# Kernel tuning notes

Hardware: AMD Instinct MI355X
Metric: run time of the kernel (lower is better)

## Reference

```python
import jax, jax.numpy as jnp
import numpy as np

B, T, C = 4, 2048, 2048
H = 16
DK = C // H // 2          # head_k_dim = 64
DV = C // H               # head_v_dim = 128
KEY_DIM = H * DK          # 1024
VAL_DIM = H * DV          # 2048
CONV = 4                  # short conv kernel size
SCALE = DK ** -0.5


def setup_inputs() -> dict:
    key = jax.random.key(0)
    ks = jax.random.split(key, 12)
    s = 0.02
    rn = lambda k, shape, sc: (jax.random.normal(k, shape) * sc).astype(jnp.float32)
    return dict(
        x=jax.random.normal(ks[0], (B, T, C), jnp.float32),
        qk_w=rn(ks[1], (2 * KEY_DIM, C), s),
        vg_w=rn(ks[2], (2 * VAL_DIM, C), s),
        o_w=rn(ks[3], (C, VAL_DIM), s),
        a_w=rn(ks[4], (H, C), s),
        b_w=rn(ks[5], (H, C), s),
        b_bias=jnp.zeros((H,), jnp.float32),
        beta_bias=jnp.linspace(-1.5, 1.5, H).astype(jnp.float32),
        A_log=jnp.log(jax.random.uniform(ks[6], (H,), minval=2.0, maxval=8.0)).astype(jnp.float32),
        dt_bias=rn(ks[7], (H,), 0.1),
        q_conv_w=rn(ks[8], (KEY_DIM, 1, CONV), 0.3),
        k_conv_w=rn(ks[9], (KEY_DIM, 1, CONV), 0.3),
        v_conv_w=rn(ks[10], (VAL_DIM, 1, CONV), 0.3),
    )


def _causal_dwconv_silu(x, w):
    # x: [B,T,Ch], w: [Ch,1,K]; Conv1d(groups=Ch, padding=K-1) truncated to T == causal conv
    y = jax.lax.conv_general_dilated(
        jnp.transpose(x, (0, 2, 1)), w, (1,), [(w.shape[-1] - 1, 0)],
        dimension_numbers=('NCH', 'OIH', 'NCH'), feature_group_count=x.shape[-1])
    return jax.nn.silu(jnp.transpose(y, (0, 2, 1)))


def _l2norm(x, eps=1e-6):
    return x * jax.lax.rsqrt(jnp.sum(x * x, axis=-1, keepdims=True) + eps)


def _gated_delta_rule(q, k, v, g, beta):
    # q,k: [B,T,H,DK], v: [B,T,H,DV], g,beta: [B,T,H]
    q = _l2norm(q) * SCALE
    k = _l2norm(k)
    # time-major for scan
    qt, kt, vt = (jnp.moveaxis(a, 1, 0) for a in (q, k, v))
    gt, bt = jnp.moveaxis(g, 1, 0), jnp.moveaxis(beta, 1, 0)

    def step(S, inp):
        q_t, k_t, v_t, g_t, b_t = inp          # S: [B,H,DK,DV]
        S = S * jnp.exp(g_t)[..., None, None]  # forget gate
        mem = jnp.einsum('bhk,bhkv->bhv', k_t, S)
        delta = (v_t - mem) * b_t[..., None]   # beta-scaled delta update
        S = S + jnp.einsum('bhk,bhv->bhkv', k_t, delta)
        o_t = jnp.einsum('bhk,bhkv->bhv', q_t, S)
        return S, o_t

    S0 = jnp.zeros((q.shape[0], H, DK, DV), q.dtype)
    _, o = jax.lax.scan(step, S0, (qt, kt, vt, gt, bt))
    return jnp.moveaxis(o, 0, 1)  # [B,T,H,DV]


def reference(x, qk_w, vg_w, o_w, a_w, b_w, b_bias, beta_bias, A_log, dt_bias,
              q_conv_w, k_conv_w, v_conv_w):
    qk = x @ qk_w.T
    vg = x @ vg_w.T
    q, k = qk[..., :KEY_DIM], qk[..., KEY_DIM:]
    v, g_out = vg[..., :VAL_DIM], vg[..., VAL_DIM:]

    q = _causal_dwconv_silu(q, q_conv_w)
    k = _causal_dwconv_silu(k, k_conv_w)
    v = _causal_dwconv_silu(v, v_conv_w)

    Bm, Tm = x.shape[0], x.shape[1]
    q = q.reshape(Bm, Tm, H, DK)
    k = k.reshape(Bm, Tm, H, DK)
    v = v.reshape(Bm, Tm, H, DV)

    beta = jax.nn.sigmoid(x @ b_w.T + b_bias + beta_bias) * 2.0          # [B,T,H]
    g = -jnp.exp(A_log) * jax.nn.softplus(x @ a_w.T + dt_bias)           # [B,T,H]

    o = _gated_delta_rule(q, k, v, g, beta)                              # [B,T,H,DV]

    eps = jnp.finfo(o.dtype).eps
    o = o * jax.lax.rsqrt(jnp.mean(o * o, axis=-1, keepdims=True) + eps)  # rms_norm (no weight)
    o = o * jax.nn.silu(g_out.reshape(Bm, Tm, H, DV))
    return o.reshape(Bm, Tm, VAL_DIM) @ o_w.T
```

## Files before the change

kernel.cpp:

```cpp
#include <hip/hip_runtime.h>
#include <hip/hip_bf16.h>
#include <stdint.h>

#define B_ 4
#define T_ 2048
#define C_ 2048
#define H_ 16
#define DK_ 64
#define DV_ 128
#define BT_ (B_ * T_)

typedef __attribute__((ext_vector_type(8))) __bf16 bf16x8;
typedef __attribute__((ext_vector_type(4))) float f32x4;

__device__ __forceinline__ unsigned short f2bf(float f) {
    union { float f; uint32_t u; } v; v.f = f;
    uint32_t u = v.u;
    uint32_t r = u + 0x7FFFu + ((u >> 16) & 1u);
    return (unsigned short)(r >> 16);
}
__device__ __forceinline__ float bf2f(unsigned short h) {
    union { uint32_t u; float f; } v; v.u = ((uint32_t)h) << 16; return v.f;
}
__device__ __forceinline__ float siluf(float x) { return x / (1.f + expf(-x)); }

__device__ __forceinline__ float dpp_xor1_add(float x) {
    int t = __builtin_amdgcn_update_dpp(0, __float_as_int(x), 0xB1, 0xF, 0xF, true);
    return x + __int_as_float(t);
}
__device__ __forceinline__ float dpp_xor2_add(float x) {
    int t = __builtin_amdgcn_update_dpp(0, __float_as_int(x), 0x4E, 0xF, 0xF, true);
    return x + __int_as_float(t);
}

__device__ __forceinline__ void split_hl(float x, unsigned short& h, unsigned short& l) {
    unsigned short hu = f2bf(x);
    float lo = x - bf2f(hu);
    h = hu;
    l = (unsigned short)(__float_as_uint(lo) >> 16);
}

__global__ void cast_split_k(const float* __restrict__ in,
                             unsigned short* __restrict__ oh, unsigned short* __restrict__ ol, int n4) {
    int i = blockIdx.x * blockDim.x + threadIdx.x;
    if (i >= n4) return;
    float4 v = ((const float4*)in)[i];
    ushort4 h, l;
    split_hl(v.x, h.x, l.x); split_hl(v.y, h.y, l.y);
    split_hl(v.z, h.z, l.z); split_hl(v.w, h.w, l.w);
    ((ushort4*)oh)[i] = h;
    ((ushort4*)ol)[i] = l;
}

__global__ void cast_plain_k(const float* __restrict__ in, unsigned short* __restrict__ out, int n4) {
    int i = blockIdx.x * blockDim.x + threadIdx.x;
    if (i >= n4) return;
    float4 v = ((const float4*)in)[i];
    ushort4 o;
    o.x = f2bf(v.x); o.y = f2bf(v.y); o.z = f2bf(v.z); o.w = f2bf(v.w);
    ((ushort4*)out)[i] = o;
}

__device__ __forceinline__ void gld_lds16(const unsigned short* gptr,
                                          unsigned short* lds_base) {
    __builtin_amdgcn_global_load_lds(
        (const __attribute__((address_space(1))) uint32_t*)(uintptr_t)gptr,
        (__attribute__((address_space(3))) uint32_t*)(uint32_t)(uintptr_t)lds_base,
        16, 0, 0);
}

template<bool DO_LO, bool F32OUT>
__global__ __launch_bounds__(256)
void gemm_bf(const unsigned short* __restrict__ Ah, const unsigned short* __restrict__ Al, int lda,
             const unsigned short* __restrict__ Wh, const unsigned short* __restrict__ Wl,
             void* __restrict__ Cout, int M, int N, int K) {
    __shared__ __align__(16) unsigned short sAh[128 * 64];
    __shared__ __align__(16) unsigned short sWh[128 * 64];
    __shared__ __align__(16) unsigned short sAl[DO_LO ? 128 * 64 : 16];
    __shared__ __align__(16) unsigned short sWl[DO_LO ? 128 * 64 : 16];
    const int tid  = threadIdx.x;
    const int wave = tid >> 6;
    const int lane = tid & 63;
    const int wm = (wave >> 1) * 64;
    const int wn = (wave & 1) * 64;
    const int bm = blockIdx.y, bn = blockIdx.x;
    const int srow = lane >> 3;
    const int scol = (lane & 7) * 8;

    const unsigned short* Agh = Ah + (size_t)(bm * 128) * lda;
    const unsigned short* Agl = DO_LO ? (Al + (size_t)(bm * 128) * lda) : nullptr;
    const unsigned short* Wgh = Wh + (size_t)(bn * 128) * K;
    const unsigned short* Wgl = DO_LO ? (Wl + (size_t)(bn * 128) * K) : nullptr;

    f32x4 acc[4][4];
#pragma unroll
    for (int i = 0; i < 4; i++)
#pragma unroll
        for (int j = 0; j < 4; j++) { acc[i][j][0]=0.f; acc[i][j][1]=0.f; acc[i][j][2]=0.f; acc[i][j][3]=0.f; }

    const int mrow = lane & 15;
    const int kq   = (lane >> 4) * 8;

    for (int k0 = 0; k0 < K; k0 += 64) {
#pragma unroll
        for (int i = 0; i < 4; i++) {
            int rbase = wave * 32 + i * 8;
            gld_lds16(Agh + (size_t)(rbase + srow) * lda + k0 + scol, sAh + rbase * 64);
            gld_lds16(Wgh + (size_t)(rbase + srow) * K   + k0 + scol, sWh + rbase * 64);
            if (DO_LO) {
                gld_lds16(Agl + (size_t)(rbase + srow) * lda + k0 + scol, sAl + rbase * 64);
                gld_lds16(Wgl + (size_t)(rbase + srow) * K   + k0 + scol, sWl + rbase * 64);
            }
        }
        __syncthreads();
#pragma unroll
        for (int kk = 0; kk < 2; kk++) {
            bf16x8 afh[4], wfh[4];
#pragma unroll
            for (int i = 0; i < 4; i++)
                afh[i] = *(const bf16x8*)(sAh + (wm + i * 16 + mrow) * 64 + kk * 32 + kq);
#pragma unroll
            for (int j = 0; j < 4; j++)
                wfh[j] = *(const bf16x8*)(sWh + (wn + j * 16 + mrow) * 64 + kk * 32 + kq);
#pragma unroll
            for (int i = 0; i < 4; i++)
#pragma unroll
                for (int j = 0; j < 4; j++)
                    acc[i][j] = __builtin_amdgcn_mfma_f32_16x16x32_bf16(afh[i], wfh[j], acc[i][j], 0, 0, 0);
            if (DO_LO) {
                bf16x8 afl[4], wfl[4];
#pragma unroll
                for (int i = 0; i < 4; i++)
                    afl[i] = *(const bf16x8*)(sAl + (wm + i * 16 + mrow) * 64 + kk * 32 + kq);
#pragma unroll
                for (int j = 0; j < 4; j++)
                    wfl[j] = *(const bf16x8*)(sWl + (wn + j * 16 + mrow) * 64 + kk * 32 + kq);
#pragma unroll
                for (int i = 0; i < 4; i++)
#pragma unroll
                    for (int j = 0; j < 4; j++) {
                        acc[i][j] = __builtin_amdgcn_mfma_f32_16x16x32_bf16(afh[i], wfl[j], acc[i][j], 0, 0, 0);
                        acc[i][j] = __builtin_amdgcn_mfma_f32_16x16x32_bf16(afl[i], wfh[j], acc[i][j], 0, 0, 0);
                    }
            }
        }
        __syncthreads();
    }
    const int r0 = (lane >> 4) * 4;
    const int cn = lane & 15;
#pragma unroll
    for (int i = 0; i < 4; i++) {
#pragma unroll
        for (int r = 0; r < 4; r++) {
            int row = bm * 128 + wm + i * 16 + r0 + r;
            size_t base = (size_t)row * N + bn * 128 + wn + cn;
            if constexpr (F32OUT) {
                float* Crow = (float*)Cout + base;
#pragma unroll
                for (int j = 0; j < 4; j++) Crow[j * 16] = acc[i][j][r];
            } else {
                unsigned short* Crow = (unsigned short*)Cout + base;
#pragma unroll
                for (int j = 0; j < 4; j++) Crow[j * 16] = f2bf(acc[i][j][r]);
            }
        }
    }
}

template<bool DO_LO, bool F32OUT, bool A_F32>
__global__ __launch_bounds__(512, 2)
void gemm_pc(const void* __restrict__ Aptr, int lda,
             const unsigned short* __restrict__ Wh, const unsigned short* __restrict__ Wl,
             void* __restrict__ Cout, int M, int N, int K) {
    __shared__ __align__(16) unsigned short sAh[2][128 * 64];
    __shared__ __align__(16) unsigned short sWh[2][128 * 64];
    __shared__ __align__(16) unsigned short sAl[DO_LO ? 2 : 1][DO_LO ? 128 * 64 : 16];
    __shared__ __align__(16) unsigned short sWl[DO_LO ? 2 : 1][DO_LO ? 128 * 64 : 16];

    const int tid  = threadIdx.x;
    const bool is_cons = (tid < 256);
    const int bm = blockIdx.y, bn = blockIdx.x;
    const int NK = K >> 6;

    const int ptid  = tid - 256;
    const int pw    = ptid >> 6;
    const int plane = ptid & 63;
    const int wrow  = plane >> 3;
    const int wcol  = (plane & 7) * 8;

    const float*          Agf = (const float*)Aptr + (size_t)(bm * 128) * lda;
    const unsigned short* Agb = (const unsigned short*)Aptr + (size_t)(bm * 128) * lda;
    const unsigned short* Whg = Wh + (size_t)(bn * 128) * K;
    const unsigned short* Wlg = DO_LO ? (Wl + (size_t)(bn * 128) * K) : nullptr;

    auto stage = [&](int p, int k0) {
#pragma unroll
        for (int i = 0; i < 4; i++) {
            int rbase = pw * 32 + i * 8;
            gld_lds16(Whg + (size_t)(rbase + wrow) * K + k0 + wcol, sWh[p] + rbase * 64);
            if (DO_LO)
                gld_lds16(Wlg + (size_t)(rbase + wrow) * K + k0 + wcol, sWl[p] + rbase * 64);
            if (!A_F32)
                gld_lds16(Agb + (size_t)(rbase + wrow) * lda + k0 + wcol, sAh[p] + rbase * 64);
        }
        if (A_F32) {
#pragma unroll
            for (int it = 0; it < 8; it++) {
                int idx = it * 256 + ptid;
                int r   = idx >> 4;
                int c4  = (idx & 15) * 4;
                float4 v = *(const float4*)(Agf + (size_t)r * lda + k0 + c4);
                ushort4 h, l;
                split_hl(v.x, h.x, l.x); split_hl(v.y, h.y, l.y);
                split_hl(v.z, h.z, l.z); split_hl(v.w, h.w, l.w);
                *(ushort4*)(sAh[p] + r * 64 + c4) = h;
                if (DO_LO) *(ushort4*)(sAl[p] + r * 64 + c4) = l;
            }
        }
    };

    const int wave = tid >> 6;
    const int lane = tid & 63;
    const int wm = (wave >> 1) * 64;
    const int wn = (wave & 1) * 64;
    const int mrow = lane & 15;
    const int kq   = (lane >> 4) * 8;

    f32x4 acc[4][4];
#pragma unroll
    for (int i = 0; i < 4; i++)
#pragma unroll
        for (int j = 0; j < 4; j++) { acc[i][j][0]=0.f; acc[i][j][1]=0.f; acc[i][j][2]=0.f; acc[i][j][3]=0.f; }

    if (!is_cons) stage(0, 0);
    __syncthreads();

    for (int ks = 0; ks < NK; ks++) {
        const int p = ks & 1;
        if (is_cons) {
            const unsigned short* pAh = sAh[p];
            const unsigned short* pWh = sWh[p];
            const unsigned short* pAl = sAl[DO_LO ? p : 0];
            const unsigned short* pWl = sWl[DO_LO ? p : 0];
#pragma unroll
            for (int kk = 0; kk < 2; kk++) {
                bf16x8 afh[4], wfh[4];
#pragma unroll
                for (int i = 0; i < 4; i++)
                    afh[i] = *(const bf16x8*)(pAh + (wm + i * 16 + mrow) * 64 + kk * 32 + kq);
#pragma unroll
                for (int j = 0; j < 4; j++)
                    wfh[j] = *(const bf16x8*)(pWh + (wn + j * 16 + mrow) * 64 + kk * 32 + kq);
#pragma unroll
                for (int i = 0; i < 4; i++)
#pragma unroll
                    for (int j = 0; j < 4; j++)
                        acc[i][j] = __builtin_amdgcn_mfma_f32_16x16x32_bf16(afh[i], wfh[j], acc[i][j], 0, 0, 0);
                if (DO_LO) {
                    bf16x8 afl[4], wfl[4];
#pragma unroll
                    for (int i = 0; i < 4; i++)
                        afl[i] = *(const bf16x8*)(pAl + (wm + i * 16 + mrow) * 64 + kk * 32 + kq);
#pragma unroll
                    for (int j = 0; j < 4; j++)
                        wfl[j] = *(const bf16x8*)(pWl + (wn + j * 16 + mrow) * 64 + kk * 32 + kq);
#pragma unroll
                    for (int i = 0; i < 4; i++)
#pragma unroll
                        for (int j = 0; j < 4; j++) {
                            acc[i][j] = __builtin_amdgcn_mfma_f32_16x16x32_bf16(afh[i], wfl[j], acc[i][j], 0, 0, 0);
                            acc[i][j] = __builtin_amdgcn_mfma_f32_16x16x32_bf16(afl[i], wfh[j], acc[i][j], 0, 0, 0);
                        }
                }
            }
        } else if (ks + 1 < NK) {
            stage(p ^ 1, (ks + 1) * 64);
        }
        __syncthreads();
    }

    if (is_cons) {
        const int r0 = (lane >> 4) * 4;
        const int cn = lane & 15;
#pragma unroll
        for (int i = 0; i < 4; i++) {
#pragma unroll
            for (int r = 0; r < 4; r++) {
                int row = bm * 128 + wm + i * 16 + r0 + r;
                size_t base = (size_t)row * N + bn * 128 + wn + cn;
                if constexpr (F32OUT) {
                    float* Crow = (float*)Cout + base;
#pragma unroll
                    for (int j = 0; j < 4; j++) Crow[j * 16] = acc[i][j][r];
                } else {
                    unsigned short* Crow = (unsigned short*)Cout + base;
#pragma unroll
                    for (int j = 0; j < 4; j++) Crow[j * 16] = f2bf(acc[i][j][r]);
                }
            }
        }
    }
}

__device__ __forceinline__ float softplusf(float x) {
    return (x > 20.f) ? x : log1pf(expf(x));
}

__global__ __launch_bounds__(256)
void gates_k(const float* __restrict__ x, const float* __restrict__ a_w, const float* __restrict__ b_w,
             const float* __restrict__ b_bias, const float* __restrict__ beta_bias,
             const float* __restrict__ A_log, const float* __restrict__ dt_bias,
             float* __restrict__ g, float* __restrict__ beta) {
    int bt = blockIdx.x;
    int wave = threadIdx.x >> 6, lane = threadIdx.x & 63;
    const float* xr = x + (size_t)bt * C_;
#pragma unroll
    for (int dd = 0; dd < 8; dd++) {
        int d = wave * 8 + dd;
        int h = d & 15;
        const float* wr = (d < 16 ? a_w : b_w) + (size_t)h * C_;
        float acc = 0.f;
#pragma unroll
        for (int it = 0; it < 8; it++) {
            float4 xv = ((const float4*)xr)[lane + it * 64];
            float4 wv = ((const float4*)wr)[lane + it * 64];
            acc += xv.x * wv.x + xv.y * wv.y + xv.z * wv.z + xv.w * wv.w;
        }
        acc += __shfl_xor(acc, 1);  acc += __shfl_xor(acc, 2);  acc += __shfl_xor(acc, 4);
        acc += __shfl_xor(acc, 8);  acc += __shfl_xor(acc, 16); acc += __shfl_xor(acc, 32);
        if (lane == 0) {
            if (d < 16) {
                g[(size_t)bt * H_ + h] = -expf(A_log[h]) * softplusf(acc + dt_bias[h]);
            } else {
                float s = 1.f / (1.f + expf(-(acc + b_bias[h] + beta_bias[h])));
                beta[(size_t)bt * H_ + h] = 2.f * s;
            }
        }
    }
}

#define CT_ 32
#define NCH_ (T_ / CT_)

#define LOAD_STEP(t2, kf, qf, vt, dec, btt)                                  \
    {                                                                        \
        _Pragma("unroll")                                                    \
        for (int u = 0; u < 4; u++) {                                        \
            float4 k4 = ((const float4*)(skp + (t2) * 68 + dk0))[u];         \
            float4 q4 = ((const float4*)(sqp + (t2) * 68 + dk0))[u];         \
            kf[u*4+0]=k4.x; kf[u*4+1]=k4.y; kf[u*4+2]=k4.z; kf[u*4+3]=k4.w;  \
            qf[u*4+0]=q4.x; qf[u*4+1]=q4.y; qf[u*4+2]=q4.z; qf[u*4+3]=q4.w;  \
        }                                                                    \
        vt  = svp[(t2) * 68 + dvl];                                          \
        dec = sgp_[(t2)];                                                    \
        btt = sbp_[(t2)];                                                    \
    }

#define DO_STEP(t2, kf, qf, vt, dec, btt)                                    \
    {                                                                        \
        float m0=0.f, m1=0.f, m2=0.f, m3=0.f;                                \
        _Pragma("unroll")                                                    \
        for (int u = 0; u < 4; u++) {                                        \
            m0 += kf[u*4+0]*S[u*4+0]; m1 += kf[u*4+1]*S[u*4+1];              \
            m2 += kf[u*4+2]*S[u*4+2]; m3 += kf[u*4+3]*S[u*4+3];              \
        }                                                                    \
        float m = (m0 + m1) + (m2 + m3);                                     \
        m = dpp_xor1_add(m);                                                 \
        m = dpp_xor2_add(m);                                                 \
        _Pragma("unroll")                                                    \
        for (int i = 0; i < 16; i++) S[i] *= dec;                            \
        float delta = (vt - m * dec) * btt;                                  \
        float o0=0.f, o1=0.f, o2=0.f, o3=0.f;                                \
        _Pragma("unroll")                                                    \
        for (int u = 0; u < 4; u++) {                                        \
            S[u*4+0] += kf[u*4+0]*delta; o0 += qf[u*4+0]*S[u*4+0];           \
            S[u*4+1] += kf[u*4+1]*delta; o1 += qf[u*4+1]*S[u*4+1];           \
            S[u*4+2] += kf[u*4+2]*delta; o2 += qf[u*4+2]*S[u*4+2];           \
            S[u*4+3] += kf[u*4+3]*delta; o3 += qf[u*4+3]*S[u*4+3];           \
        }                                                                    \
        float ov = (o0 + o1) + (o2 + o3);                                    \
        ov = dpp_xor1_add(ov);                                               \
        ov = dpp_xor2_add(ov);                                               \
        if (dkq == 0)                                                        \
            vbuf[vbase + (size_t)(tc + (t2)) * 2048 + dvl] = ov;             \
    }

#define CONSUME_GROUP(TB, TE)                                                \
    {                                                                        \
        float kfa[16], qfa[16], kfb[16], qfb[16];                            \
        float vta, deca, btta, vtb, decb, bttb;                              \
        LOAD_STEP(TB, kfa, qfa, vta, deca, btta);                            \
        int t2 = TB;                                                         \
        _Pragma("unroll 1")                                                  \
        for (; t2 + 2 <= (TE); t2 += 2) {                                    \
            LOAD_STEP(t2 + 1, kfb, qfb, vtb, decb, bttb);                    \
            DO_STEP(t2, kfa, qfa, vta, deca, btta);                          \
            if (t2 + 2 < (TE))                                               \
                LOAD_STEP(t2 + 2, kfa, qfa, vta, deca, btta);                \
            DO_STEP(t2 + 1, kfb, qfb, vtb, decb, bttb);                      \
        }                                                                    \
        if (t2 < (TE))                                                       \
            DO_STEP(t2, kfa, qfa, vta, deca, btta);                          \
    }

__global__ __launch_bounds__(512)
void scan_fused(const float* __restrict__ qk, float* __restrict__ vbuf,
                const float* __restrict__ qcw, const float* __restrict__ kcw, const float* __restrict__ vcw,
                const float* __restrict__ g, const float* __restrict__ beta) {
    int blk = blockIdx.x;
    int vh  = blk & 1;
    int bh  = blk >> 1;
    int b   = bh >> 4;
    int h   = bh & 15;
    int tid = threadIdx.x;

    __shared__ __align__(16) float rawq[2][(CT_ + 3) * 64];
    __shared__ __align__(16) float rawk[2][(CT_ + 3) * 64];
    __shared__ __align__(16) float rawv[2][(CT_ + 3) * 64];
    __shared__ __align__(16) float sq[2][CT_ * 68];
    __shared__ __align__(16) float sk[2][CT_ * 68];
    __shared__ __align__(16) float sv[2][CT_ * 68];
    __shared__ float sg[2][CT_];
    __shared__ float sb[2][CT_];

    const size_t qbase = (size_t)b * T_ * 2048 + h * 64;
    const size_t kbase = qbase + 1024;
    const size_t vbase = (size_t)b * T_ * 2048 + h * 128 + vh * 64;
    const size_t gbase = (size_t)b * T_ * H_ + h;

    const bool is_cons = (tid < 256);

    const int ptid = tid - 256;
    const int pc   = ptid & 63;
    const int pw   = ptid >> 6;
    float wqa[4], wka[4], wva[4];
    if (!is_cons) {
        float4 a4 = *(const float4*)(qcw + (size_t)(h * 64 + pc) * 4);
        float4 b4 = *(const float4*)(kcw + (size_t)(h * 64 + pc) * 4);
        float4 c4 = *(const float4*)(vcw + (size_t)(h * 128 + vh * 64 + pc) * 4);
        wqa[0]=a4.x; wqa[1]=a4.y; wqa[2]=a4.z; wqa[3]=a4.w;
        wka[0]=b4.x; wka[1]=b4.y; wka[2]=b4.z; wka[3]=b4.w;
        wva[0]=c4.x; wva[1]=c4.y; wva[2]=c4.z; wva[3]=c4.w;
        if (ptid < 192) {
            int bsel = ptid >> 6, c = ptid & 63;
            float* rb = bsel == 0 ? rawq[1] : (bsel == 1 ? rawk[1] : rawv[1]);
#pragma unroll
            for (int j = 0; j < 3; j++) rb[(CT_ + j) * 64 + c] = 0.f;
        }
    }

    auto prod_phase1 = [&](int ci) {
        int rp = ci & 1;
        int tcc = ci * CT_;
        float* rq = rawq[rp]; float* rk = rawk[rp]; float* rv = rawv[rp];
        const float* pq = rawq[rp ^ 1]; const float* pk = rawk[rp ^ 1]; const float* pv = rawv[rp ^ 1];
        if (ptid < 192) {
            int bsel = ptid >> 6, c = ptid & 63;
            float*       db = bsel == 0 ? rq : (bsel == 1 ? rk : rv);
            const float* sc = bsel == 0 ? pq : (bsel == 1 ? pk : pv);
#pragma unroll
            for (int j = 0; j < 3; j++) db[j * 64 + c] = sc[(CT_ + j) * 64 + c];
        }
#pragma unroll
        for (int u = 0; u < 2; u++) {
            int idx = u * 256 + ptid;
            int r   = idx >> 4;
            int c4  = (idx & 15) * 4;
            size_t row = (size_t)(tcc + r) * 2048;
            *(float4*)(rq + (3 + r) * 64 + c4) = *(const float4*)(qk + qbase + row + c4);
            *(float4*)(rk + (3 + r) * 64 + c4) = *(const float4*)(qk + kbase + row + c4);
            *(float4*)(rv + (3 + r) * 64 + c4) = *(const float4*)(vbuf + vbase + row + c4);
        }
        if (ptid < CT_)          sg[rp][ptid]       = expf(g[gbase + (size_t)(tcc + ptid) * H_]);
        else if (ptid < 2 * CT_) sb[rp][ptid - CT_] = beta[gbase + (size_t)(tcc + ptid - CT_) * H_];
    };

    auto prod_phase2 = [&](int ci) {
        int rp = ci & 1;
        const float* rq = rawq[rp]; const float* rk = rawk[rp]; const float* rv = rawv[rp];
        float* dq = sq[rp]; float* dk = sk[rp]; float* dv = sv[rp];
#pragma unroll
        for (int it = 0; it < 8; it++) {
            int r = pw + it * 4;
            float aq = 0.f, ak = 0.f, av = 0.f;
#pragma unroll
            for (int j = 0; j < 4; j++) {
                aq += wqa[j] * rq[(r + j) * 64 + pc];
                ak += wka[j] * rk[(r + j) * 64 + pc];
                av += wva[j] * rv[(r + j) * 64 + pc];
            }
            dq[r * 68 + pc] = siluf(aq);
            dk[r * 68 + pc] = siluf(ak);
            dv[r * 68 + pc] = siluf(av);
        }
    };

    auto prod_phase3 = [&](int ci) {
        int rp = ci & 1;
        int r = ptid >> 3;
        int j = ptid & 7;
        float* kr = sk[rp] + r * 68 + j * 8;
        float* qr = sq[rp] + r * 68 + j * 8;
        float4 k0 = ((const float4*)kr)[0], k1 = ((const float4*)kr)[1];
        float4 q0 = ((const float4*)qr)[0], q1 = ((const float4*)qr)[1];
        float ssk = k0.x*k0.x + k0.y*k0.y + k0.z*k0.z + k0.w*k0.w
                  + k1.x*k1.x + k1.y*k1.y + k1.z*k1.z + k1.w*k1.w;
        float ssq = q0.x*q0.x + q0.y*q0.y + q0.z*q0.z + q0.w*q0.w
                  + q1.x*q1.x + q1.y*q1.y + q1.z*q1.z + q1.w*q1.w;
        ssk += __shfl_xor(ssk, 1); ssk += __shfl_xor(ssk, 2); ssk += __shfl_xor(ssk, 4);
        ssq += __shfl_xor(ssq, 1); ssq += __shfl_xor(ssq, 2); ssq += __shfl_xor(ssq, 4);
        float rk_ = rsqrtf(ssk + 1e-6f);
        float rq_ = rsqrtf(ssq + 1e-6f) * 0.125f;
        k0.x*=rk_; k0.y*=rk_; k0.z*=rk_; k0.w*=rk_;
        k1.x*=rk_; k1.y*=rk_; k1.z*=rk_; k1.w*=rk_;
        q0.x*=rq_; q0.y*=rq_; q0.z*=rq_; q0.w*=rq_;
        q1.x*=rq_; q1.y*=rq_; q1.z*=rq_; q1.w*=rq_;
        ((float4*)kr)[0] = k0; ((float4*)kr)[1] = k1;
        ((float4*)qr)[0] = q0; ((float4*)qr)[1] = q1;
    };

    const int dkq = tid & 3;
    const int dvl = tid >> 2;
    const int dk0 = dkq * 16;
    float S[16];
#pragma unroll
    for (int i = 0; i < 16; i++) S[i] = 0.f;

    if (!is_cons) prod_phase1(0);
    __syncthreads();
    if (!is_cons) prod_phase2(0);
    __syncthreads();
    if (!is_cons) prod_phase3(0);
    __syncthreads();

    for (int ci = 0; ci < NCH_; ci++) {
        const int p  = ci & 1;
        const int tc = ci * CT_;
        const float* sqp  = sq[p];
        const float* skp  = sk[p];
        const float* svp  = sv[p];
        const float* sgp_ = sg[p];
        const float* sbp_ = sb[p];

        if (is_cons) { CONSUME_GROUP(0, 11); }
        else if (ci + 1 < NCH_) prod_phase1(ci + 1);
        __syncthreads();
        if (is_cons) { CONSUME_GROUP(11, 22); }
        else if (ci + 1 < NCH_) prod_phase2(ci + 1);
        __syncthreads();
        if (is_cons) { CONSUME_GROUP(22, 32); }
        else if (ci + 1 < NCH_) prod_phase3(ci + 1);
        __syncthreads();
    }
}

__global__ __launch_bounds__(256)
void postnorm_k(float* __restrict__ vbuf, const unsigned short* __restrict__ gout) {
    int bt  = blockIdx.x;
    int tid = threadIdx.x;
    const float* orow = vbuf + (size_t)bt * 2048 + tid * 8;
    float4 a = ((const float4*)orow)[0];
    float4 c = ((const float4*)orow)[1];
    float ss = a.x*a.x + a.y*a.y + a.z*a.z + a.w*a.w
             + c.x*c.x + c.y*c.y + c.z*c.z + c.w*c.w;
    ss += __shfl_xor(ss, 1); ss += __shfl_xor(ss, 2); ss += __shfl_xor(ss, 4); ss += __shfl_xor(ss, 8);
    float rms = rsqrtf(ss * (1.f / 128.f) + 1.1920928955078125e-07f);
    const unsigned short* grow = gout + (size_t)bt * 2048 + tid * 8;
    ushort4 g1 = ((const ushort4*)grow)[0];
    ushort4 g2 = ((const ushort4*)grow)[1];
    ushort4 r0, r1;
    r0.x = f2bf(a.x * rms * siluf(bf2f(g1.x)));
    r0.y = f2bf(a.y * rms * siluf(bf2f(g1.y)));
    r0.z = f2bf(a.z * rms * siluf(bf2f(g1.z)));
    r0.w = f2bf(a.w * rms * siluf(bf2f(g1.w)));
    r1.x = f2bf(c.x * rms * siluf(bf2f(g2.x)));
    r1.y = f2bf(c.y * rms * siluf(bf2f(g2.y)));
    r1.z = f2bf(c.z * rms * siluf(bf2f(g2.z)));
    r1.w = f2bf(c.w * rms * siluf(bf2f(g2.w)));
    __syncthreads();
    unsigned short* og = (unsigned short*)vbuf + (size_t)bt * 4096 + tid * 8;
    *(ushort4*)og       = r0;
    *(ushort4*)(og + 4) = r1;
}

extern "C" void kernel_launch(void* const* d_in, const int* in_sizes, int n_in,
                              void* d_out, int out_size, void* d_ws, size_t ws_size,
                              hipStream_t stream) {
    (void)in_sizes; (void)n_in; (void)out_size;
    const float* x        = (const float*)d_in[0];
    const float* qk_w     = (const float*)d_in[1];
    const float* vg_w     = (const float*)d_in[2];
    const float* o_w      = (const float*)d_in[3];
    const float* a_w      = (const float*)d_in[4];
    const float* b_w      = (const float*)d_in[5];
    const float* b_bias   = (const float*)d_in[6];
    const float* beta_b   = (const float*)d_in[7];
    const float* A_log    = (const float*)d_in[8];
    const float* dt_bias  = (const float*)d_in[9];
    const float* q_conv_w = (const float*)d_in[10];
    const float* k_conv_w = (const float*)d_in[11];
    const float* v_conv_w = (const float*)d_in[12];

    char* ws = (char*)d_ws;
    float* qkf            = (float*)d_out;
    unsigned short* goutb = (unsigned short*)d_out;
    float* outp           = (float*)d_out;

    if (ws_size >= (size_t)177u * 1024u * 1024u) {
        unsigned short* xh    = (unsigned short*)(ws);
        unsigned short* xl    = (unsigned short*)(ws + (32u << 20));
        unsigned short* qkw_h = (unsigned short*)(ws + (64u << 20));
        unsigned short* qkw_l = (unsigned short*)(ws + (72u << 20));
        unsigned short* vgw_h = (unsigned short*)(ws + (80u << 20));
        unsigned short* vgw_l = (unsigned short*)(ws + (96u << 20));
        unsigned short* ow_bf = (unsigned short*)(ws + (104u << 20));
        float*          vbuf  = (float*)(ws + (112u << 20));
        float*          gbuf  = (float*)(ws + (176u << 20));
        float*          bbuf  = (float*)(ws + (176u << 20) + (512u << 10));

        cast_split_k<<<(BT_ * C_ / 4 + 255) / 256, 256, 0, stream>>>(x, xh, xl, BT_ * C_ / 4);
        cast_split_k<<<(2048 * 2048 / 4 + 255) / 256, 256, 0, stream>>>(qk_w, qkw_h, qkw_l, 2048 * 2048 / 4);
        cast_split_k<<<(2048 * 2048 / 4 + 255) / 256, 256, 0, stream>>>(vg_w, vgw_h, vgw_l, 2048 * 2048 / 4);
        cast_plain_k<<<(2048 * 2048 / 4 + 255) / 256, 256, 0, stream>>>(
            vg_w + (size_t)2048 * 2048, vgw_h + (size_t)2048 * 2048, 2048 * 2048 / 4);
        cast_plain_k<<<(2048 * 2048 / 4 + 255) / 256, 256, 0, stream>>>(o_w, ow_bf, 2048 * 2048 / 4);

        gemm_bf<true, true><<<dim3(16, 64), 256, 0, stream>>>(xh, xl, 2048, qkw_h, qkw_l, qkf, BT_, 2048, 2048);
        gemm_bf<true, true><<<dim3(16, 64), 256, 0, stream>>>(xh, xl, 2048, vgw_h, vgw_l, vbuf, BT_, 2048, 2048);

        gates_k<<<BT_, 256, 0, stream>>>(x, a_w, b_w, b_bias, beta_b, A_log, dt_bias, gbuf, bbuf);

        scan_fused<<<B_ * H_ * 2, 512, 0, stream>>>(qkf, vbuf, q_conv_w, k_conv_w, v_conv_w, gbuf, bbuf);

        gemm_bf<false, false><<<dim3(16, 64), 256, 0, stream>>>(
            xh, nullptr, 2048, vgw_h + (size_t)2048 * 2048, nullptr, goutb, BT_, 2048, 2048);

        postnorm_k<<<BT_, 256, 0, stream>>>(vbuf, goutb);

        gemm_bf<false, true><<<dim3(16, 64), 256, 0, stream>>>(
            (const unsigned short*)vbuf, nullptr, 4096, ow_bf, nullptr, outp, BT_, 2048, 2048);
    } else {
        unsigned short* qkw_h = (unsigned short*)(ws);
        unsigned short* qkw_l = (unsigned short*)(ws + (8u  << 20));
        unsigned short* vgw_h = (unsigned short*)(ws + (16u << 20));
        unsigned short* vgw_l = (unsigned short*)(ws + (32u << 20));
        unsigned short* ow_bf = (unsigned short*)(ws + (48u << 20));
        float*          vbuf  = (float*)(ws + (56u << 20));
        float*          gbuf  = (float*)(ws + (120u << 20));
        float*          bbuf  = (float*)(ws + (120u << 20) + (512u << 10));

        cast_split_k<<<(2048 * 2048 / 4 + 255) / 256, 256, 0, stream>>>(qk_w, qkw_h, qkw_l, 2048 * 2048 / 4);
        cast_split_k<<<(2048 * 2048 / 4 + 255) / 256, 256, 0, stream>>>(vg_w, vgw_h, vgw_l, 2048 * 2048 / 4);
        cast_plain_k<<<(2048 * 2048 / 4 + 255) / 256, 256, 0, stream>>>(
            vg_w + (size_t)2048 * 2048, vgw_h + (size_t)2048 * 2048, 2048 * 2048 / 4);
        cast_plain_k<<<(2048 * 2048 / 4 + 255) / 256, 256, 0, stream>>>(o_w, ow_bf, 2048 * 2048 / 4);

        gemm_pc<true, true, true><<<dim3(16, 64), 512, 0, stream>>>(x, 2048, qkw_h, qkw_l, qkf, BT_, 2048, 2048);
        gemm_pc<true, true, true><<<dim3(16, 64), 512, 0, stream>>>(x, 2048, vgw_h, vgw_l, vbuf, BT_, 2048, 2048);

        gates_k<<<BT_, 256, 0, stream>>>(x, a_w, b_w, b_bias, beta_b, A_log, dt_bias, gbuf, bbuf);

        scan_fused<<<B_ * H_ * 2, 512, 0, stream>>>(qkf, vbuf, q_conv_w, k_conv_w, v_conv_w, gbuf, bbuf);

        gemm_pc<false, false, true><<<dim3(16, 64), 512, 0, stream>>>(
            x, 2048, vgw_h + (size_t)2048 * 2048, nullptr, goutb, BT_, 2048, 2048);

        postnorm_k<<<BT_, 256, 0, stream>>>(vbuf, goutb);

        gemm_pc<false, true, false><<<dim3(16, 64), 512, 0, stream>>>(
            (const void*)vbuf, 4096, ow_bf, nullptr, outp, BT_, 2048, 2048);
    }
}
```

Before: 1.483 ms.

## Overlap gate GEMM with scan in one launch and merge casts and QK/VG GEMMs

Merges the five cast kernels into a single launch. Merges the qk and vg split-precision GEMMs into one dual-output grid. Fuses the scan with the g_out GEMM in one heterogeneous launch: the first 128 blocks run the recurrent scan and the remaining 1024 blocks run the bf16 gate GEMM. The scan only fills 128 blocks, so the goal is to use the idle CUs during the long sequential scan and to save launch overhead. The trade-off is that the combined kernel uses dynamic shared memory sized for the scan, and g_out now aliases the xl buffer, which must not be needed after the first GEMM.

```diff
diff --git a/kernel.cpp b/kernel.cpp
--- a/kernel.cpp
+++ b/kernel.cpp
@@ -59,6 +59,35 @@
     ushort4 o;
     o.x = f2bf(v.x); o.y = f2bf(v.y); o.z = f2bf(v.z); o.w = f2bf(v.w);
     ((ushort4*)out)[i] = o;
+}
+
+__global__ __launch_bounds__(256)
+void cast_all_k(const float* __restrict__ x, const float* __restrict__ qk_w,
+                const float* __restrict__ vg_w, const float* __restrict__ o_w,
+                unsigned short* __restrict__ xh, unsigned short* __restrict__ xl,
+                unsigned short* __restrict__ qkw_h, unsigned short* __restrict__ qkw_l,
+                unsigned short* __restrict__ vgw_h, unsigned short* __restrict__ vgw_l,
+                unsigned short* __restrict__ ow_bf) {
+    const int NX = BT_ * C_ / 4;
+    const int NW = 2048 * 2048 / 4;
+    int i = blockIdx.x * blockDim.x + threadIdx.x;
+    const float* src; unsigned short *dh, *dl; int j; bool split;
+    if (i < NX)               { j = i;            src = x;                          dh = xh;    dl = xl;    split = true; }
+    else if (i < NX + NW)     { j = i - NX;       src = qk_w;                       dh = qkw_h; dl = qkw_l; split = true; }
+    else if (i < NX + 2 * NW) { j = i - NX - NW;  src = vg_w;                       dh = vgw_h; dl = vgw_l; split = true; }
+    else if (i < NX + 3 * NW) { j = i - NX - 2*NW; src = vg_w + (size_t)2048*2048;  dh = vgw_h + (size_t)2048*2048; dl = nullptr; split = false; }
+    else                      { j = i - NX - 3*NW; src = o_w;                       dh = ow_bf; dl = nullptr; split = false; }
+    float4 v = ((const float4*)src)[j];
+    ushort4 h, l;
+    if (split) {
+        split_hl(v.x, h.x, l.x); split_hl(v.y, h.y, l.y);
+        split_hl(v.z, h.z, l.z); split_hl(v.w, h.w, l.w);
+        ((ushort4*)dh)[j] = h;
+        ((ushort4*)dl)[j] = l;
+    } else {
+        h.x = f2bf(v.x); h.y = f2bf(v.y); h.z = f2bf(v.z); h.w = f2bf(v.w);
+        ((ushort4*)dh)[j] = h;
+    }
 }
 
 __device__ __forceinline__ void gld_lds16(const unsigned short* gptr,
@@ -163,6 +192,98 @@
 #pragma unroll
                 for (int j = 0; j < 4; j++) Crow[j * 16] = f2bf(acc[i][j][r]);
             }
+        }
+    }
+}
+
+__global__ __launch_bounds__(256)
+void gemm_dual(const unsigned short* __restrict__ Ah, const unsigned short* __restrict__ Al,
+               const unsigned short* __restrict__ Wh0, const unsigned short* __restrict__ Wl0, float* __restrict__ C0,
+               const unsigned short* __restrict__ Wh1, const unsigned short* __restrict__ Wl1, float* __restrict__ C1) {
+    __shared__ __align__(16) unsigned short sAh[128 * 64];
+    __shared__ __align__(16) unsigned short sWh[128 * 64];
+    __shared__ __align__(16) unsigned short sAl[128 * 64];
+    __shared__ __align__(16) unsigned short sWl[128 * 64];
+    const int K = 2048, N = 2048, lda = 2048;
+    const int tid  = threadIdx.x;
+    const int wave = tid >> 6;
+    const int lane = tid & 63;
+    const int wm = (wave >> 1) * 64;
+    const int wn = (wave & 1) * 64;
+    const int bm = blockIdx.y;
+    const int bnx = blockIdx.x;
+    const unsigned short* Wh = (bnx < 16) ? Wh0 : Wh1;
+    const unsigned short* Wl = (bnx < 16) ? Wl0 : Wl1;
+    float* Csel              = (bnx < 16) ? C0  : C1;
+    const int bn = bnx & 15;
+    const int srow = lane >> 3;
+    const int scol = (lane & 7) * 8;
+
+    const unsigned short* Agh = Ah + (size_t)(bm * 128) * lda;
+    const unsigned short* Agl = Al + (size_t)(bm * 128) * lda;
+    const unsigned short* Wgh = Wh + (size_t)(bn * 128) * K;
+    const unsigned short* Wgl = Wl + (size_t)(bn * 128) * K;
+
+    f32x4 acc[4][4];
+#pragma unroll
+    for (int i = 0; i < 4; i++)
+#pragma unroll
+        for (int j = 0; j < 4; j++) { acc[i][j][0]=0.f; acc[i][j][1]=0.f; acc[i][j][2]=0.f; acc[i][j][3]=0.f; }
+
+    const int mrow = lane & 15;
+    const int kq   = (lane >> 4) * 8;
+
+    for (int k0 = 0; k0 < K; k0 += 64) {
+#pragma unroll
+        for (int i = 0; i < 4; i++) {
+            int rbase = wave * 32 + i * 8;
+            gld_lds16(Agh + (size_t)(rbase + srow) * lda + k0 + scol, sAh + rbase * 64);
+            gld_lds16(Wgh + (size_t)(rbase + srow) * K   + k0 + scol, sWh + rbase * 64);
+            gld_lds16(Agl + (size_t)(rbase + srow) * lda + k0 + scol, sAl + rbase * 64);
+            gld_lds16(Wgl + (size_t)(rbase + srow) * K   + k0 + scol, sWl + rbase * 64);
+        }
+        __syncthreads();
+#pragma unroll
+        for (int kk = 0; kk < 2; kk++) {
+            bf16x8 afh[4], wfh[4];
+#pragma unroll
+            for (int i = 0; i < 4; i++)
+                afh[i] = *(const bf16x8*)(sAh + (wm + i * 16 + mrow) * 64 + kk * 32 + kq);
+#pragma unroll
+            for (int j = 0; j < 4; j++)
+                wfh[j] = *(const bf16x8*)(sWh + (wn + j * 16 + mrow) * 64 + kk * 32 + kq);
+#pragma unroll
+            for (int i = 0; i < 4; i++)
+#pragma unroll
+                for (int j = 0; j < 4; j++)
+                    acc[i][j] = __builtin_amdgcn_mfma_f32_16x16x32_bf16(afh[i], wfh[j], acc[i][j], 0, 0, 0);
+            bf16x8 afl[4], wfl[4];
+#pragma unroll
+            for (int i = 0; i < 4; i++)
+                afl[i] = *(const bf16x8*)(sAl + (wm + i * 16 + mrow) * 64 + kk * 32 + kq);
+#pragma unroll
+            for (int j = 0; j < 4; j++)
+                wfl[j] = *(const bf16x8*)(sWl + (wn + j * 16 + mrow) * 64 + kk * 32 + kq);
+#pragma unroll
+            for (int i = 0; i < 4; i++)
+#pragma unroll
+                for (int j = 0; j < 4; j++) {
+                    acc[i][j] = __builtin_amdgcn_mfma_f32_16x16x32_bf16(afh[i], wfl[j], acc[i][j], 0, 0, 0);
+                    acc[i][j] = __builtin_amdgcn_mfma_f32_16x16x32_bf16(afl[i], wfh[j], acc[i][j], 0, 0, 0);
+                }
+        }
+        __syncthreads();
+    }
+    const int r0 = (lane >> 4) * 4;
+    const int cn = lane & 15;
+#pragma unroll
+    for (int i = 0; i < 4; i++) {
+#pragma unroll
+        for (int r = 0; r < 4; r++) {
+            int row = bm * 128 + wm + i * 16 + r0 + r;
+            float* Crow = Csel + (size_t)row * N + bn * 128 + wn + cn;
+#pragma unroll
+            for (int j = 0; j < 4; j++) Crow[j * 16] = acc[i][j][r];
         }
     }
 }
@@ -403,6 +524,215 @@
             DO_STEP(t2, kfa, qfa, vta, deca, btta);                          \
     }
 
+__global__ __launch_bounds__(512, 4)
+void scan_gemm_k(const float* __restrict__ qk, float* __restrict__ vbuf,
+                 const float* __restrict__ qcw, const float* __restrict__ kcw, const float* __restrict__ vcw,
+                 const float* __restrict__ g, const float* __restrict__ beta,
+                 const unsigned short* __restrict__ xh, const unsigned short* __restrict__ gwh,
+                 unsigned short* __restrict__ gout) {
+    extern __shared__ char smem_raw[];
+    const int blk = blockIdx.x;
+    const int tid = threadIdx.x;
+
+    if (blk >= 128) {
+        const int bid = blk - 128;
+        const int bm = bid >> 4;
+        const int bn = bid & 15;
+        unsigned short* sA = (unsigned short*)smem_raw;
+        unsigned short* sB = sA + 128 * 64;
+        const bool act = tid < 256;
+        const int wave = tid >> 6;
+        const int lane = tid & 63;
+        const int wm = (wave >> 1) * 64;
+        const int wn = (wave & 1) * 64;
+        const int srow = lane >> 3;
+        const int scol = (lane & 7) * 8;
+        const int mrow = lane & 15;
+        const int kq   = (lane >> 4) * 8;
+        const unsigned short* Ag = xh  + (size_t)(bm * 128) * 2048;
+        const unsigned short* Wg = gwh + (size_t)(bn * 128) * 2048;
+        f32x4 acc[4][4];
+#pragma unroll
+        for (int i = 0; i < 4; i++)
+#pragma unroll
+            for (int j = 0; j < 4; j++) { acc[i][j][0]=0.f; acc[i][j][1]=0.f; acc[i][j][2]=0.f; acc[i][j][3]=0.f; }
+        for (int k0 = 0; k0 < 2048; k0 += 64) {
+            if (act) {
+#pragma unroll
+                for (int i = 0; i < 4; i++) {
+                    int rbase = wave * 32 + i * 8;
+                    gld_lds16(Ag + (size_t)(rbase + srow) * 2048 + k0 + scol, sA + rbase * 64);
+                    gld_lds16(Wg + (size_t)(rbase + srow) * 2048 + k0 + scol, sB + rbase * 64);
+                }
+            }
+            __syncthreads();
+            if (act) {
+#pragma unroll
+                for (int kk = 0; kk < 2; kk++) {
+                    bf16x8 af[4], bfr[4];
+#pragma unroll
+                    for (int i = 0; i < 4; i++)
+                        af[i] = *(const bf16x8*)(sA + (wm + i * 16 + mrow) * 64 + kk * 32 + kq);
+#pragma unroll
+                    for (int j = 0; j < 4; j++)
+                        bfr[j] = *(const bf16x8*)(sB + (wn + j * 16 + mrow) * 64 + kk * 32 + kq);
+#pragma unroll
+                    for (int i = 0; i < 4; i++)
+#pragma unroll
+                        for (int j = 0; j < 4; j++)
+                            acc[i][j] = __builtin_amdgcn_mfma_f32_16x16x32_bf16(af[i], bfr[j], acc[i][j], 0, 0, 0);
+                }
+            }
+            __syncthreads();
+        }
+        if (act) {
+            const int r0 = (lane >> 4) * 4;
+            const int cn = lane & 15;
+#pragma unroll
+            for (int i = 0; i < 4; i++) {
+#pragma unroll
+                for (int r = 0; r < 4; r++) {
+                    int row = bm * 128 + wm + i * 16 + r0 + r;
+                    unsigned short* Crow = gout + (size_t)row * 2048 + bn * 128 + wn + cn;
+#pragma unroll
+                    for (int j = 0; j < 4; j++) Crow[j * 16] = f2bf(acc[i][j][r]);
+                }
+            }
+        }
+        return;
+    }
+
+    const int vh  = blk & 1;
+    const int bh  = blk >> 1;
+    const int b   = bh >> 4;
+    const int h   = bh & 15;
+
+    float* sqb  = (float*)smem_raw;
+    float* skb  = sqb + 2 * CT_ * 68;
+    float* svb  = skb + 2 * CT_ * 68;
+    float* sgb  = svb + 2 * CT_ * 68;
+    float* sbb  = sgb + 2 * CT_;
+    float* vcar = sbb + 2 * CT_;
+
+    const size_t qbase = (size_t)b * T_ * 2048 + h * 64;
+    const size_t kbase = qbase + 1024;
+    const size_t vbase = (size_t)b * T_ * 2048 + h * 128 + vh * 64;
+    const size_t gbase = (size_t)b * T_ * H_ + h;
+
+    const bool is_cons = (tid < 256);
+
+    const int ptid = tid - 256;
+    const int pc   = ptid & 63;
+    const int pw   = ptid >> 6;
+    const int R0   = pw * 8;
+    float wqa[4], wka[4], wva[4];
+    if (!is_cons) {
+        float4 a4 = *(const float4*)(qcw + (size_t)(h * 64 + pc) * 4);
+        float4 b4 = *(const float4*)(kcw + (size_t)(h * 64 + pc) * 4);
+        float4 c4 = *(const float4*)(vcw + (size_t)(h * 128 + vh * 64 + pc) * 4);
+        wqa[0]=a4.x; wqa[1]=a4.y; wqa[2]=a4.z; wqa[3]=a4.w;
+        wka[0]=b4.x; wka[1]=b4.y; wka[2]=b4.z; wka[3]=b4.w;
+        wva[0]=c4.x; wva[1]=c4.y; wva[2]=c4.z; wva[3]=c4.w;
+    }
+
+    auto stage = [&](int ci) {
+        const int rp  = ci & 1;
+        const int tcc = ci * CT_;
+        float* dq = sqb + rp * (CT_ * 68);
+        float* dk = skb + rp * (CT_ * 68);
+        float* dv = svb + rp * (CT_ * 68);
+        float qin[11], kin[11], vin[11];
+#pragma unroll
+        for (int j = 0; j < 11; j++) {
+            int rr = tcc + R0 - 3 + j;
+            bool ok = (rr >= 0);
+            qin[j] = ok ? qk[qbase + (size_t)rr * 2048 + pc] : 0.f;
+            kin[j] = ok ? qk[kbase + (size_t)rr * 2048 + pc] : 0.f;
+        }
+        if (pw == 0) {
+#pragma unroll
+            for (int j = 0; j < 3; j++) vin[j] = vcar[(rp ^ 1) * 192 + j * 64 + pc];
+#pragma unroll
+            for (int j = 3; j < 11; j++) vin[j] = vbuf[vbase + (size_t)(tcc + j - 3) * 2048 + pc];
+        } else {
+#pragma unroll
+            for (int j = 0; j < 11; j++) vin[j] = vbuf[vbase + (size_t)(tcc + R0 - 3 + j) * 2048 + pc];
+        }
+        if (pw == 3) {
+#pragma unroll
+            for (int j = 0; j < 3; j++) vcar[rp * 192 + j * 64 + pc] = vin[8 + j];
+        }
+#pragma unroll
+        for (int it = 0; it < 8; it++) {
+            const int r = R0 + it;
+            float aq = 0.f, ak = 0.f, av = 0.f;
+#pragma unroll
+            for (int j = 0; j < 4; j++) {
+                aq += wqa[j] * qin[it + j];
+                ak += wka[j] * kin[it + j];
+                av += wva[j] * vin[it + j];
+            }
+            dq[r * 68 + pc] = siluf(aq);
+            dk[r * 68 + pc] = siluf(ak);
+            dv[r * 68 + pc] = siluf(av);
+        }
+        if (ptid < CT_)          sgb[rp * CT_ + ptid]       = expf(g[gbase + (size_t)(tcc + ptid) * H_]);
+        else if (ptid < 2 * CT_) sbb[rp * CT_ + ptid - CT_] = beta[gbase + (size_t)(tcc + ptid - CT_) * H_];
+        {
+            const int rl = R0 + (pc >> 3);
+            const int jc = pc & 7;
+            float* kr = dk + rl * 68 + jc * 8;
+            float* qr = dq + rl * 68 + jc * 8;
+            float4 k0 = ((const float4*)kr)[0], k1 = ((const float4*)kr)[1];
+            float4 q0 = ((const float4*)qr)[0], q1 = ((const float4*)qr)[1];
+            float ssk = k0.x*k0.x + k0.y*k0.y + k0.z*k0.z + k0.w*k0.w
+                      + k1.x*k1.x + k1.y*k1.y + k1.z*k1.z + k1.w*k1.w;
+            float ssq = q0.x*q0.x + q0.y*q0.y + q0.z*q0.z + q0.w*q0.w
+                      + q1.x*q1.x + q1.y*q1.y + q1.z*q1.z + q1.w*q1.w;
+            ssk += __shfl_xor(ssk, 1); ssk += __shfl_xor(ssk, 2); ssk += __shfl_xor(ssk, 4);
+            ssq += __shfl_xor(ssq, 1); ssq += __shfl_xor(ssq, 2); ssq += __shfl_xor(ssq, 4);
+            float rk_ = rsqrtf(ssk + 1e-6f);
+            float rq_ = rsqrtf(ssq + 1e-6f) * 0.125f;
+            k0.x*=rk_; k0.y*=rk_; k0.z*=rk_; k0.w*=rk_;
+            k1.x*=rk_; k1.y*=rk_; k1.z*=rk_; k1.w*=rk_;
+            q0.x*=rq_; q0.y*=rq_; q0.z*=rq_; q0.w*=rq_;
+            q1.x*=rq_; q1.y*=rq_; q1.z*=rq_; q1.w*=rq_;
+            ((float4*)kr)[0] = k0; ((float4*)kr)[1] = k1;
+            ((float4*)qr)[0] = q0; ((float4*)qr)[1] = q1;
+        }
+    };
+
+    const int dkq = tid & 3;
+    const int dvl = tid >> 2;
+    const int dk0 = dkq * 16;
+    float S[16];
+#pragma unroll
+    for (int i = 0; i < 16; i++) S[i] = 0.f;
+
+    if (!is_cons) {
+        if (pw == 0) {
+#pragma unroll
+            for (int j = 0; j < 3; j++) vcar[192 + j * 64 + pc] = 0.f;
+        }
+        stage(0);
+    }
+    __syncthreads();
+
+    for (int ci = 0; ci < NCH_; ci++) {
+        const int p  = ci & 1;
+        const int tc = ci * CT_;
+        const float* sqp  = sqb + p * (CT_ * 68);
+        const float* skp  = skb + p * (CT_ * 68);
+        const float* svp  = svb + p * (CT_ * 68);
+        const float* sgp_ = sgb + p * CT_;
+        const float* sbp_ = sbb + p * CT_;
+
+        if (is_cons) { CONSUME_GROUP(0, CT_); }
+        else if (ci + 1 < NCH_) stage(ci + 1);
+        __syncthreads();
+    }
+}
+
 __global__ __launch_bounds__(512)
 void scan_fused(const float* __restrict__ qk, float* __restrict__ vbuf,
                 const float* __restrict__ qcw, const float* __restrict__ kcw, const float* __restrict__ vcw,
@@ -603,7 +933,6 @@
 
     char* ws = (char*)d_ws;
     float* qkf            = (float*)d_out;
-    unsigned short* goutb = (unsigned short*)d_out;
     float* outp           = (float*)d_out;
 
     if (ws_size >= (size_t)177u * 1024u * 1024u) {
@@ -617,23 +946,21 @@
         float*          vbuf  = (float*)(ws + (112u << 20));
         float*          gbuf  = (float*)(ws + (176u << 20));
         float*          bbuf  = (float*)(ws + (176u << 20) + (512u << 10));
-
-        cast_split_k<<<(BT_ * C_ / 4 + 255) / 256, 256, 0, stream>>>(x, xh, xl, BT_ * C_ / 4);
-        cast_split_k<<<(2048 * 2048 / 4 + 255) / 256, 256, 0, stream>>>(qk_w, qkw_h, qkw_l, 2048 * 2048 / 4);
-        cast_split_k<<<(2048 * 2048 / 4 + 255) / 256, 256, 0, stream>>>(vg_w, vgw_h, vgw_l, 2048 * 2048 / 4);
-        cast_plain_k<<<(2048 * 2048 / 4 + 255) / 256, 256, 0, stream>>>(
-            vg_w + (size_t)2048 * 2048, vgw_h + (size_t)2048 * 2048, 2048 * 2048 / 4);
-        cast_plain_k<<<(2048 * 2048 / 4 + 255) / 256, 256, 0, stream>>>(o_w, ow_bf, 2048 * 2048 / 4);
-
-        gemm_bf<true, true><<<dim3(16, 64), 256, 0, stream>>>(xh, xl, 2048, qkw_h, qkw_l, qkf, BT_, 2048, 2048);
-        gemm_bf<true, true><<<dim3(16, 64), 256, 0, stream>>>(xh, xl, 2048, vgw_h, vgw_l, vbuf, BT_, 2048, 2048);
+        unsigned short* goutb = xl;
+
+        {
+            const int NTOT = BT_ * C_ / 4 + 4 * (2048 * 2048 / 4);
+            cast_all_k<<<NTOT / 256, 256, 0, stream>>>(x, qk_w, vg_w, o_w,
+                xh, xl, qkw_h, qkw_l, vgw_h, vgw_l, ow_bf);
+        }
+
+        gemm_dual<<<dim3(32, 64), 256, 0, stream>>>(xh, xl, qkw_h, qkw_l, qkf, vgw_h, vgw_l, vbuf);
 
         gates_k<<<BT_, 256, 0, stream>>>(x, a_w, b_w, b_bias, beta_b, A_log, dt_bias, gbuf, bbuf);
 
-        scan_fused<<<B_ * H_ * 2, 512, 0, stream>>>(qkf, vbuf, q_conv_w, k_conv_w, v_conv_w, gbuf, bbuf);
-
-        gemm_bf<false, false><<<dim3(16, 64), 256, 0, stream>>>(
-            xh, nullptr, 2048, vgw_h + (size_t)2048 * 2048, nullptr, goutb, BT_, 2048, 2048);
+        scan_gemm_k<<<128 + 1024, 512, 54272, stream>>>(
+            qkf, vbuf, q_conv_w, k_conv_w, v_conv_w, gbuf, bbuf,
+            xh, vgw_h + (size_t)2048 * 2048, goutb);
 
         postnorm_k<<<BT_, 256, 0, stream>>>(vbuf, goutb);
 
@@ -648,6 +975,7 @@
         float*          vbuf  = (float*)(ws + (56u << 20));
         float*          gbuf  = (float*)(ws + (120u << 20));
         float*          bbuf  = (float*)(ws + (120u << 20) + (512u << 10));
+        unsigned short* goutb = (unsigned short*)d_out;
 
         cast_split_k<<<(2048 * 2048 / 4 + 255) / 256, 256, 0, stream>>>(qk_w, qkw_h, qkw_l, 2048 * 2048 / 4);
         cast_split_k<<<(2048 * 2048 / 4 + 255) / 256, 256, 0, stream>>>(vg_w, vgw_h, vgw_l, 2048 * 2048 / 4);
```

Measured after the change: 1.358 ms. 8.4% less time.
